# Optimization experiments

Measured on AMD Instinct MI355X. Metric: run time of the kernel, lower is better.

Reference implementation:

```python
import jax, jax.numpy as jnp
import numpy as np

B, T, D, H = 8, 512, 1024, 16
DK = D // H          # 64
S = 2 * T - 1        # 1023 relative positions


def setup_inputs() -> dict:
    key = jax.random.key(0)
    ks = jax.random.split(key, 10)
    s = 0.02
    return {
        "x": jax.random.normal(ks[0], (B, T, D), jnp.float32),
        "mask": jax.random.randint(ks[1], (B, T, T), 0, 2) > 0,
        "pos": jax.random.normal(ks[2], (1, S, D), jnp.float32),
        "Wqkv": jax.random.normal(ks[3], (3 * D, D), jnp.float32) * s,
        "bqkv": jnp.zeros((3 * D,), jnp.float32),
        "Wpos": jax.random.normal(ks[4], (D, D), jnp.float32) * s,
        "posu": jax.random.normal(ks[5], (1, 1, H, DK), jnp.float32) * s,
        "posv": jax.random.normal(ks[6], (1, 1, H, DK), jnp.float32) * s,
        "Wout": jax.random.normal(ks[7], (D, D), jnp.float32) * s,
        "bout": jnp.zeros((D,), jnp.float32),
    }


def reference(x, mask, pos, Wqkv, bqkv, Wpos, posu, posv, Wout, bout):
    # QKV projection and head split
    qkv = x @ Wqkv.T + bqkv                               # [B,T,3D]
    q, k, v = jnp.split(qkv, 3, axis=-1)
    q = q.reshape(B, T, H, DK)                            # [B,T,H,dk]
    k = k.reshape(B, T, H, DK).transpose(0, 2, 1, 3)      # [B,H,T,dk]
    v = v.reshape(B, T, H, DK).transpose(0, 2, 1, 3)      # [B,H,T,dk]
    # positional projection (no bias)
    p = (pos @ Wpos.T).reshape(1, S, H, DK).transpose(0, 2, 1, 3)  # [1,H,S,dk]
    # content (AC) and position (BD) terms
    q_u = (q + posu).transpose(0, 2, 1, 3)                # [B,H,T,dk]
    q_v = (q + posv).transpose(0, 2, 1, 3)                # [B,H,T,dk]
    AC = jnp.einsum('bhtd,bhsd->bhts', q_u, k)            # [B,H,T,T]
    matrix_bd = jnp.einsum('bhtd,zhsd->bhts', q_v, p)     # [B,H,T,S]
    # Transformer-XL style relative gather: index (j - i) + (T-1)
    r = jnp.arange(T)
    rel = (r[None, :] - r[:, None]) + (T - 1)             # [T,T], values in [0, S)
    BD = jnp.take_along_axis(matrix_bd, rel[None, None], axis=3)  # [B,H,T,T]
    scores = (AC + BD) / jnp.sqrt(jnp.float32(DK))
    scores = jnp.where(mask[:, None], scores, jnp.float32(-100000.0))
    weights = jax.nn.softmax(scores, axis=-1)             # [B,H,T,T]
    ctx = jnp.einsum('bhts,bhsd->bthd', weights, v).reshape(B, T, D)
    out = ctx @ Wout.T + bout                             # dropout rate 0 -> identity
    return out, weights
```

## Files before the change

### kernel.cpp

```cpp
#include <hip/hip_runtime.h>

#define BB 8
#define TT 512
#define DD 1024
#define HH 16
#define DKK 64
#define SS 1023

typedef unsigned short u16;
typedef __attribute__((ext_vector_type(8))) short bf16x8;
typedef __attribute__((ext_vector_type(4))) float f32x4;

#define MFMA16(a, b, c) __builtin_amdgcn_mfma_f32_16x16x32_bf16((a), (b), (c), 0, 0, 0)

__device__ __forceinline__ float us2f(u16 u) {
    unsigned int x = ((unsigned int)u) << 16;
    return __uint_as_float(x);
}
__device__ __forceinline__ u16 f2us(float f) {
    unsigned int x = __float_as_uint(f);
    unsigned int lsb = (x >> 16) & 1u;
    x += 0x7fffu + lsb;
    return (u16)(x >> 16);
}
__device__ __forceinline__ bf16x8 cvt8(const float* p) {
    float4 f1 = *(const float4*)p;
    float4 f2 = *(const float4*)(p + 4);
    bf16x8 r;
    r[0] = (short)f2us(f1.x); r[1] = (short)f2us(f1.y);
    r[2] = (short)f2us(f1.z); r[3] = (short)f2us(f1.w);
    r[4] = (short)f2us(f2.x); r[5] = (short)f2us(f2.y);
    r[6] = (short)f2us(f2.z); r[7] = (short)f2us(f2.w);
    return r;
}

__global__ void detect_kernel(const u16* __restrict__ w,
                              const unsigned int* __restrict__ mask,
                              int* __restrict__ flags) {
    if (threadIdx.x == 0 && blockIdx.x == 0) {
        int plaus = 0;
        for (int i = 0; i < 256; i++) {
            u16 hw = w[i];
            int e = (hw >> 7) & 0xFF;
            if (e == 0 || (e >= 87 && e <= 131)) plaus++;
        }
        flags[0] = (plaus >= 205) ? 1 : 0;
        int ok = 1;
        for (int i = 0; i < 64; i++) if (mask[i] > 1u) ok = 0;
        flags[1] = ok;
    }
}

template<int OMODE>
__global__ __launch_bounds__(256) void gemm_mfma(
    const void* __restrict__ Av, const void* __restrict__ Wv,
    const void* __restrict__ bias, const int* __restrict__ flags,
    float* __restrict__ qT, u16* __restrict__ kB, u16* __restrict__ vB,
    u16* __restrict__ pB, void* __restrict__ oout, int M, int N, int K)
{
    const bool isbf = (flags[0] != 0);
    __shared__ u16 As[64][40];
    __shared__ u16 Bs[64][40];
    const int tid = threadIdx.x;
    const int w = tid >> 6, lane = tid & 63;
    const int quad = lane >> 4, l16 = lane & 15;
    const int bn = blockIdx.x * 64, bm = blockIdx.y * 64;
    const int srow = tid >> 2;
    const int koff = (tid & 3) * 8;
    const int garow = (OMODE == 1) ? min(bm + srow, M - 1) : (bm + srow);
    const int gbrow = bn + srow;

    f32x4 C[4];
    #pragma unroll
    for (int i = 0; i < 4; i++) { C[i][0] = 0.f; C[i][1] = 0.f; C[i][2] = 0.f; C[i][3] = 0.f; }

    for (int k0 = 0; k0 < K; k0 += 32) {
        bf16x8 av, bv;
        if (OMODE == 2) {
            const int kk = k0 + koff;
            const float* ap = qT + (((size_t)((garow >> 9) * HH + (kk >> 6)) * TT + (garow & 511)) << 6) + (kk & 63);
            av = cvt8(ap);
        } else if (isbf) {
            av = *(const bf16x8*)((const u16*)Av + (size_t)garow * K + k0 + koff);
        } else {
            av = cvt8((const float*)Av + (size_t)garow * K + k0 + koff);
        }
        if (isbf) {
            bv = *(const bf16x8*)((const u16*)Wv + (size_t)gbrow * K + k0 + koff);
        } else {
            bv = cvt8((const float*)Wv + (size_t)gbrow * K + k0 + koff);
        }

        __syncthreads();
        *(bf16x8*)&As[srow][koff] = av;
        *(bf16x8*)&Bs[srow][koff] = bv;
        __syncthreads();

        bf16x8 af = *(const bf16x8*)&As[w * 16 + l16][quad * 8];
        #pragma unroll
        for (int ct = 0; ct < 4; ct++) {
            bf16x8 bf = *(const bf16x8*)&Bs[ct * 16 + l16][quad * 8];
            C[ct] = MFMA16(af, bf, C[ct]);
        }
    }

    #pragma unroll
    for (int ct = 0; ct < 4; ct++) {
        #pragma unroll
        for (int r = 0; r < 4; r++) {
            const int i = bm + w * 16 + quad * 4 + r;
            const int n = bn + ct * 16 + l16;
            float val = C[ct][r];
            if (OMODE == 0) {
                val += isbf ? us2f(((const u16*)bias)[n]) : ((const float*)bias)[n];
                const int sec = n >> 10, w_ = n & 1023;
                const int h_ = w_ >> 6, d_ = w_ & 63;
                const size_t bh_ = (size_t)((i >> 9) * HH + h_);
                const int t_ = i & 511;
                if (sec == 0) qT[((bh_ * TT + t_) << 6) + d_] = val;
                else if (sec == 1) kB[((bh_ * TT + t_) << 6) + d_] = f2us(val);
                else vB[((bh_ * DKK + d_) << 9) + t_] = f2us(val);
            } else if (OMODE == 1) {
                if (i < M) {
                    const int h_ = n >> 6, d_ = n & 63;
                    pB[((size_t)(h_ * 1024 + i) << 6) + d_] = f2us(val);
                }
            } else {
                val += isbf ? us2f(((const u16*)bias)[n]) : ((const float*)bias)[n];
                if (isbf) ((u16*)oout)[(size_t)i * N + n] = f2us(val);
                else ((float*)oout)[(size_t)i * N + n] = val;
            }
        }
    }
}

__global__ __launch_bounds__(256) void attn_mfma(
    float* __restrict__ qT, const u16* __restrict__ kB, const u16* __restrict__ vB,
    const u16* __restrict__ pB, const void* __restrict__ posu,
    const void* __restrict__ posv, const void* __restrict__ mask,
    void* __restrict__ d_out, const int* __restrict__ flags)
{
    const int t0 = blockIdx.x << 6;
    const int h = blockIdx.y, b = blockIdx.z;
    const int tid = threadIdx.x;
    const int w = tid >> 6, lane = tid & 63;
    const int quad = lane >> 4, l16 = lane & 15;
    const bool isbf = (flags[0] != 0), m32 = (flags[1] != 0);
    const size_t bh = (size_t)b * HH + h;

    __shared__ u16 wls[4][16][520];
    u16* wme = &wls[w][0][0];
    float* bdw = (float*)wme;

    const int myrow = t0 + w * 16 + l16;
    const float* qrow = qT + ((bh * TT + myrow) << 6);
    bf16x8 aU[2], aV[2];
    #pragma unroll
    for (int f = 0; f < 2; f++) {
        const int d0 = f * 32 + quad * 8;
        float q8[8], pu8[8], pv8[8];
        *(float4*)&q8[0] = *(const float4*)(qrow + d0);
        *(float4*)&q8[4] = *(const float4*)(qrow + d0 + 4);
        if (isbf) {
            const u16* puP = (const u16*)posu + h * 64 + d0;
            const u16* pvP = (const u16*)posv + h * 64 + d0;
            #pragma unroll
            for (int j = 0; j < 8; j++) { pu8[j] = us2f(puP[j]); pv8[j] = us2f(pvP[j]); }
        } else {
            const float* puP = (const float*)posu + h * 64 + d0;
            const float* pvP = (const float*)posv + h * 64 + d0;
            #pragma unroll
            for (int j = 0; j < 8; j++) { pu8[j] = puP[j]; pv8[j] = pvP[j]; }
        }
        #pragma unroll
        for (int j = 0; j < 8; j++) {
            aU[f][j] = (short)f2us((q8[j] + pu8[j]) * 0.125f);
            aV[f][j] = (short)f2us((q8[j] + pv8[j]) * 0.125f);
        }
    }

    f32x4 S[32];
    #pragma unroll
    for (int ct = 0; ct < 32; ct++) { S[ct][0] = 0.f; S[ct][1] = 0.f; S[ct][2] = 0.f; S[ct][3] = 0.f; }
    const u16* kbase = kB + ((bh * TT) << 6) + quad * 8;
    #pragma unroll
    for (int ct = 0; ct < 32; ct++) {
        const u16* kp = kbase + ((size_t)(ct * 16 + l16) << 6);
        bf16x8 b0 = *(const bf16x8*)kp;
        bf16x8 b1 = *(const bf16x8*)(kp + 32);
        S[ct] = MFMA16(aU[0], b0, S[ct]);
        S[ct] = MFMA16(aU[1], b1, S[ct]);
    }

    const u16* pbaseh = pB + ((size_t)h << 16);
    for (int g = 0; g < 8; g++) {
        const int pb = g * 64 - t0 + 496 - w * 16;
        #pragma unroll
        for (int c5 = 0; c5 < 5; c5++) {
            const u16* pp = pbaseh + ((size_t)(pb + c5 * 16 + l16) << 6) + quad * 8;
            bf16x8 b0 = *(const bf16x8*)pp;
            bf16x8 b1 = *(const bf16x8*)(pp + 32);
            f32x4 c; c[0] = 0.f; c[1] = 0.f; c[2] = 0.f; c[3] = 0.f;
            c = MFMA16(aV[0], b0, c);
            c = MFMA16(aV[1], b1, c);
            #pragma unroll
            for (int r = 0; r < 4; r++)
                bdw[(quad * 4 + r) * 84 + c5 * 16 + l16] = c[r];
        }
        __syncthreads();
        #pragma unroll
        for (int f = 0; f < 4; f++) {
            const int sc = f * 16 + l16;
            #pragma unroll
            for (int r = 0; r < 4; r++) {
                const int local = quad * 4 + r;
                S[g * 4 + f][r] += bdw[local * 83 + sc + 15];
            }
        }
        __syncthreads();
    }

    const int trow = t0 + w * 16 + quad * 4;
    #pragma unroll
    for (int ct = 0; ct < 32; ct++) {
        #pragma unroll
        for (int r = 0; r < 4; r++) {
            const size_t midx = (((size_t)b * TT + trow + r) << 9) + ct * 16 + l16;
            const int mv = m32 ? ((const int*)mask)[midx]
                               : (int)((const signed char*)mask)[midx];
            if (mv == 0) S[ct][r] = -100000.0f;
        }
    }

    float mx[4] = {-3.0e38f, -3.0e38f, -3.0e38f, -3.0e38f};
    float sm[4] = {0.f, 0.f, 0.f, 0.f};
    #pragma unroll
    for (int ct = 0; ct < 32; ct++)
        #pragma unroll
        for (int r = 0; r < 4; r++) mx[r] = fmaxf(mx[r], S[ct][r]);
    #pragma unroll
    for (int r = 0; r < 4; r++)
        #pragma unroll
        for (int off = 1; off < 16; off <<= 1) mx[r] = fmaxf(mx[r], __shfl_xor(mx[r], off, 64));
    #pragma unroll
    for (int ct = 0; ct < 32; ct++)
        #pragma unroll
        for (int r = 0; r < 4; r++) {
            float e = __expf(S[ct][r] - mx[r]);
            S[ct][r] = e;
            sm[r] += e;
        }
    #pragma unroll
    for (int r = 0; r < 4; r++) {
        #pragma unroll
        for (int off = 1; off < 16; off <<= 1) sm[r] += __shfl_xor(sm[r], off, 64);
        sm[r] = 1.0f / sm[r];
    }

    __syncthreads();
    const size_t wbase = (size_t)BB * TT * DD + (((bh * TT + trow)) << 9) + l16;
    #pragma unroll
    for (int ct = 0; ct < 32; ct++) {
        #pragma unroll
        for (int r = 0; r < 4; r++) {
            const float wv = S[ct][r] * sm[r];
            const u16 u = f2us(wv);
            wls[w][quad * 4 + r][ct * 16 + l16] = u;
            if (isbf) ((u16*)d_out)[wbase + ((size_t)r << 9) + ct * 16] = u;
            else ((float*)d_out)[wbase + ((size_t)r << 9) + ct * 16] = wv;
        }
    }
    __syncthreads();

    f32x4 Cv[4];
    #pragma unroll
    for (int i = 0; i < 4; i++) { Cv[i][0] = 0.f; Cv[i][1] = 0.f; Cv[i][2] = 0.f; Cv[i][3] = 0.f; }
    const u16* vb0 = vB + ((bh * DKK) << 9) + quad * 8;
    #pragma unroll
    for (int ks = 0; ks < 16; ks++) {
        bf16x8 aw = *(const bf16x8*)&wls[w][l16][ks * 32 + quad * 8];
        #pragma unroll
        for (int ctd = 0; ctd < 4; ctd++) {
            const u16* vp = vb0 + ((size_t)(ctd * 16 + l16) << 9) + ks * 32;
            bf16x8 bv = *(const bf16x8*)vp;
            Cv[ctd] = MFMA16(aw, bv, Cv[ctd]);
        }
    }
    float* crow = qT + ((bh * TT + trow) << 6) + l16;
    #pragma unroll
    for (int ctd = 0; ctd < 4; ctd++)
        #pragma unroll
        for (int r = 0; r < 4; r++)
            crow[(r << 6) + ctd * 16] = Cv[ctd][r];
}

extern "C" void kernel_launch(void* const* d_in, const int* in_sizes, int n_in,
                              void* d_out, int out_size, void* d_ws, size_t ws_size,
                              hipStream_t stream)
{
    const void* x    = d_in[0];
    const void* mask = d_in[1];
    const void* pos  = d_in[2];
    const void* Wqkv = d_in[3];
    const void* bqkv = d_in[4];
    const void* Wpos = d_in[5];
    const void* posu = d_in[6];
    const void* posv = d_in[7];
    const void* Wout = d_in[8];
    const void* bout = d_in[9];

    char* ws = (char*)d_ws;
    float* qT    = (float*)(ws + 0);
    u16*   kB    = (u16*)(ws + 16777216);
    u16*   vB    = (u16*)(ws + 25165824);
    u16*   pB    = (u16*)(ws + 33554432);
    int*   flags = (int*)(ws + 35651584);

    detect_kernel<<<1, 64, 0, stream>>>((const u16*)Wqkv, (const unsigned int*)mask, flags);

    gemm_mfma<0><<<dim3(48, 64), 256, 0, stream>>>(
        x, Wqkv, bqkv, flags, qT, kB, vB, pB, nullptr, BB * TT, 3 * DD, DD);

    gemm_mfma<1><<<dim3(16, 16), 256, 0, stream>>>(
        pos, Wpos, nullptr, flags, qT, kB, vB, pB, nullptr, SS, DD, DD);

    attn_mfma<<<dim3(8, HH, BB), 256, 0, stream>>>(
        qT, kB, vB, pB, posu, posv, mask, d_out, flags);

    gemm_mfma<2><<<dim3(16, 64), 256, 0, stream>>>(
        nullptr, Wout, bout, flags, qT, kB, vB, pB, d_out, BB * TT, DD, DD);
}
```

Before: 526.3 us.

## Bit-pack the mask, use wave-local sync, and vectorize bf16 weight stores

Adds a pre-pass kernel that packs the boolean mask into 32-bit words per row and lane group. Each attention block then reads one word per row instead of re-reading the full mask for every head. Block-wide __syncthreads around the per-wave shared-memory scratch become a wave-local LDS waitcnt plus a scheduling barrier, since each wave touches only its own region. In the bf16 output path, the attention weights are written out from LDS with 16-byte vector stores instead of scattered 2-byte stores. The risks are an extra kernel launch and correctness relying on waves never sharing LDS rows.

Measured after the change: 501.7 us. 4.7% less time.

```diff
diff --git a/kernel.cpp b/kernel.cpp
--- a/kernel.cpp
+++ b/kernel.cpp
@@ -12,6 +12,8 @@
 typedef __attribute__((ext_vector_type(4))) float f32x4;
 
 #define MFMA16(a, b, c) __builtin_amdgcn_mfma_f32_16x16x32_bf16((a), (b), (c), 0, 0, 0)
+
+#define WAVE_SYNC() do { asm volatile("s_waitcnt lgkmcnt(0)" ::: "memory"); __builtin_amdgcn_sched_barrier(0); } while (0)
 
 __device__ __forceinline__ float us2f(u16 u) {
     unsigned int x = ((unsigned int)u) << 16;
@@ -49,6 +51,25 @@
         for (int i = 0; i < 64; i++) if (mask[i] > 1u) ok = 0;
         flags[1] = ok;
     }
+}
+
+__global__ __launch_bounds__(256) void pack_mask(const void* __restrict__ mask,
+                                                 unsigned int* __restrict__ packed,
+                                                 const int* __restrict__ flags) {
+    const int idx = blockIdx.x * 256 + threadIdx.x;
+    const int g = idx & 15;
+    const size_t bt = (size_t)(idx >> 4);
+    unsigned int bits = 0;
+    if (flags[1]) {
+        const int* mp = (const int*)mask + bt * TT + g;
+        #pragma unroll
+        for (int k = 0; k < 32; k++) if (mp[k * 16] != 0) bits |= (1u << k);
+    } else {
+        const signed char* mp = (const signed char*)mask + bt * TT + g;
+        #pragma unroll
+        for (int k = 0; k < 32; k++) if (mp[k * 16] != 0) bits |= (1u << k);
+    }
+    packed[idx] = bits;
 }
 
 template<int OMODE>
@@ -137,7 +158,7 @@
 __global__ __launch_bounds__(256) void attn_mfma(
     float* __restrict__ qT, const u16* __restrict__ kB, const u16* __restrict__ vB,
     const u16* __restrict__ pB, const void* __restrict__ posu,
-    const void* __restrict__ posv, const void* __restrict__ mask,
+    const void* __restrict__ posv, const unsigned int* __restrict__ pmask,
     void* __restrict__ d_out, const int* __restrict__ flags)
 {
     const int t0 = blockIdx.x << 6;
@@ -145,12 +166,18 @@
     const int tid = threadIdx.x;
     const int w = tid >> 6, lane = tid & 63;
     const int quad = lane >> 4, l16 = lane & 15;
-    const bool isbf = (flags[0] != 0), m32 = (flags[1] != 0);
+    const bool isbf = (flags[0] != 0);
     const size_t bh = (size_t)b * HH + h;
 
     __shared__ u16 wls[4][16][520];
     u16* wme = &wls[w][0][0];
     float* bdw = (float*)wme;
+
+    const int trow = t0 + w * 16 + quad * 4;
+    unsigned int mrow[4];
+    #pragma unroll
+    for (int r = 0; r < 4; r++)
+        mrow[r] = pmask[((size_t)(b * TT + trow + r) << 4) + l16];
 
     const int myrow = t0 + w * 16 + l16;
     const float* qrow = qT + ((bh * TT + myrow) << 6);
@@ -207,7 +234,7 @@
             for (int r = 0; r < 4; r++)
                 bdw[(quad * 4 + r) * 84 + c5 * 16 + l16] = c[r];
         }
-        __syncthreads();
+        WAVE_SYNC();
         #pragma unroll
         for (int f = 0; f < 4; f++) {
             const int sc = f * 16 + l16;
@@ -217,18 +244,13 @@
                 S[g * 4 + f][r] += bdw[local * 83 + sc + 15];
             }
         }
-        __syncthreads();
-    }
-
-    const int trow = t0 + w * 16 + quad * 4;
+    }
+
     #pragma unroll
     for (int ct = 0; ct < 32; ct++) {
         #pragma unroll
         for (int r = 0; r < 4; r++) {
-            const size_t midx = (((size_t)b * TT + trow + r) << 9) + ct * 16 + l16;
-            const int mv = m32 ? ((const int*)mask)[midx]
-                               : (int)((const signed char*)mask)[midx];
-            if (mv == 0) S[ct][r] = -100000.0f;
+            if (!(mrow[r] & (1u << ct))) S[ct][r] = -100000.0f;
         }
     }
 
@@ -257,20 +279,26 @@
         sm[r] = 1.0f / sm[r];
     }
 
-    __syncthreads();
     const size_t wbase = (size_t)BB * TT * DD + (((bh * TT + trow)) << 9) + l16;
     #pragma unroll
     for (int ct = 0; ct < 32; ct++) {
         #pragma unroll
         for (int r = 0; r < 4; r++) {
             const float wv = S[ct][r] * sm[r];
-            const u16 u = f2us(wv);
-            wls[w][quad * 4 + r][ct * 16 + l16] = u;
-            if (isbf) ((u16*)d_out)[wbase + ((size_t)r << 9) + ct * 16] = u;
-            else ((float*)d_out)[wbase + ((size_t)r << 9) + ct * 16] = wv;
-        }
-    }
-    __syncthreads();
+            wls[w][quad * 4 + r][ct * 16 + l16] = f2us(wv);
+            if (!isbf) ((float*)d_out)[wbase + ((size_t)r << 9) + ct * 16] = wv;
+        }
+    }
+    WAVE_SYNC();
+    if (isbf) {
+        u16* wout = (u16*)d_out + (size_t)BB * TT * DD + ((bh * TT + t0 + w * 16) << 9);
+        const int lane8 = lane * 8;
+        #pragma unroll
+        for (int rr = 0; rr < 16; rr++) {
+            bf16x8 vv = *(const bf16x8*)&wls[w][rr][lane8];
+            *(bf16x8*)(wout + ((size_t)rr << 9) + lane8) = vv;
+        }
+    }
 
     f32x4 Cv[4];
     #pragma unroll
@@ -315,8 +343,10 @@
     u16*   vB    = (u16*)(ws + 25165824);
     u16*   pB    = (u16*)(ws + 33554432);
     int*   flags = (int*)(ws + 35651584);
+    unsigned int* pmask = (unsigned int*)(ws + 35655680);
 
     detect_kernel<<<1, 64, 0, stream>>>((const u16*)Wqkv, (const unsigned int*)mask, flags);
+    pack_mask<<<dim3(256), 256, 0, stream>>>(mask, pmask, flags);
 
     gemm_mfma<0><<<dim3(48, 64), 256, 0, stream>>>(
         x, Wqkv, bqkv, flags, qT, kB, vB, pB, nullptr, BB * TT, 3 * DD, DD);
@@ -325,7 +355,7 @@
         pos, Wpos, nullptr, flags, qT, kB, vB, pB, nullptr, SS, DD, DD);
 
     attn_mfma<<<dim3(8, HH, BB), 256, 0, stream>>>(
-        qT, kB, vB, pB, posu, posv, mask, d_out, flags);
+        qT, kB, vB, pB, posu, posv, pmask, d_out, flags);
 
     gemm_mfma<2><<<dim3(16, 64), 256, 0, stream>>>(
         nullptr, Wout, bout, flags, qT, kB, vB, pB, d_out, BB * TT, DD, DD);
```
